# Optimization experiments

Measured on AMD Instinct MI355X. Metric: run time of the kernel, lower is better.

The kernel has to match this reference:

```python
import jax, jax.numpy as jnp
import numpy as np

N_NODES = 50000
NEG_SLOPE = 0.2
EPS = 1e-16


def _gat_layer(x, src, dst, W, a_src, a_dst, b, concat):
    """One PyG-style GATConv layer (eval mode, self-loops already in src/dst).
    x: [N, F_in], W: [F_in, H*C], a_src/a_dst: [H, C], b: [H*C] or [C].
    """
    H, C = a_src.shape
    N = x.shape[0]
    h = (x @ W).reshape(N, H, C)                      # [N, H, C]
    alpha_s = jnp.einsum('nhc,hc->nh', h, a_src)      # [N, H]
    alpha_d = jnp.einsum('nhc,hc->nh', h, a_dst)      # [N, H]
    e = alpha_s[src] + alpha_d[dst]                   # [E, H]
    e = jax.nn.leaky_relu(e, NEG_SLOPE)
    # segment softmax over edges grouped by destination node
    m = jax.ops.segment_max(e, dst, num_segments=N)   # [N, H]
    e = jnp.exp(e - m[dst])
    denom = jax.ops.segment_sum(e, dst, num_segments=N)
    alpha = e / (denom[dst] + EPS)                    # [E, H]
    msg = h[src] * alpha[:, :, None]                  # [E, H, C]
    out = jax.ops.segment_sum(msg, dst, num_segments=N)  # [N, H, C]
    if concat:
        out = out.reshape(N, H * C)
    else:
        out = out.mean(axis=1)
    return out + b


def setup_inputs() -> dict:
    key = jax.random.key(0)
    ks = jax.random.split(key, 16)
    N, E = N_NODES, 800000
    in_dim, hid, heads = 128, 64, 2
    x = jax.random.normal(ks[0], (N, in_dim), dtype=jnp.float32)
    edge_index = jax.random.randint(ks[1], (2, E), 0, N, dtype=jnp.int64)
    s = 0.1
    return {
        'x': x,
        'edge_index': edge_index,
        # layer 0: in_dim -> hid, heads
        'W0': s * jax.random.normal(ks[2], (in_dim, heads * hid), dtype=jnp.float32),
        'as0': s * jax.random.normal(ks[3], (heads, hid), dtype=jnp.float32),
        'ad0': s * jax.random.normal(ks[4], (heads, hid), dtype=jnp.float32),
        'b0': jnp.zeros((heads * hid,), dtype=jnp.float32),
        # layer 1: hid*heads -> hid, heads
        'W1': s * jax.random.normal(ks[5], (heads * hid, heads * hid), dtype=jnp.float32),
        'as1': s * jax.random.normal(ks[6], (heads, hid), dtype=jnp.float32),
        'ad1': s * jax.random.normal(ks[7], (heads, hid), dtype=jnp.float32),
        'b1': jnp.zeros((heads * hid,), dtype=jnp.float32),
        # layer 2: hid*heads -> hid, heads=1
        'W2': s * jax.random.normal(ks[8], (heads * hid, hid), dtype=jnp.float32),
        'as2': s * jax.random.normal(ks[9], (1, hid), dtype=jnp.float32),
        'ad2': s * jax.random.normal(ks[10], (1, hid), dtype=jnp.float32),
        'b2': jnp.zeros((hid,), dtype=jnp.float32),
    }


def reference(x, edge_index, W0, as0, ad0, b0, W1, as1, ad1, b1, W2, as2, ad2, b2):
    N = x.shape[0]
    # PyG GATConv default add_self_loops=True
    loop = jnp.arange(N, dtype=edge_index.dtype)
    src = jnp.concatenate([edge_index[0], loop])
    dst = jnp.concatenate([edge_index[1], loop])
    h = _gat_layer(x, src, dst, W0, as0, ad0, b0, concat=True)
    h = jax.nn.relu(h)
    h = _gat_layer(h, src, dst, W1, as1, ad1, b1, concat=True)
    h = jax.nn.relu(h)
    out = _gat_layer(h, src, dst, W2, as2, ad2, b2, concat=True)  # heads=1: concat == identity
    return out
```

## Files before the change

kernel.cpp:

```cpp
#include <hip/hip_runtime.h>
#include <hip/hip_fp16.h>

#define NEG_SLOPE 0.2f
#define EPSF 1e-16f

template<int BN, int HEADS, bool OUTH, typename XT>
__global__ __launch_bounds__(256) void gemm_fused(const XT* __restrict__ X,
                                                  const float* __restrict__ W,
                                                  const float* __restrict__ asrc,
                                                  const float* __restrict__ adst,
                                                  float* __restrict__ OutF,
                                                  __half* __restrict__ OutH,
                                                  float* __restrict__ AS,
                                                  float* __restrict__ AD, int N) {
    constexpr int BM = 64, BK = 32, K = 128;
    constexpr int TN = BN / 16;
    __shared__ float Xs[BM][BK + 4];
    __shared__ float Ws[BK][BN];
    const int tid = threadIdx.x;
    const int tx = tid & 15, ty = tid >> 4;
    const int row0 = blockIdx.x * BM;

    float acc[4][TN];
#pragma unroll
    for (int i = 0; i < 4; ++i)
#pragma unroll
        for (int j = 0; j < TN; ++j) acc[i][j] = 0.f;

    for (int kb = 0; kb < K; kb += BK) {
        __syncthreads();
        for (int idx = tid; idx < BK * (BN / 4); idx += 256) {
            int r = idx / (BN / 4), c4 = idx % (BN / 4);
            ((float4*)&Ws[r][0])[c4] = ((const float4*)&W[(size_t)(kb + r) * BN])[c4];
        }
        for (int t = tid; t < BM * (BK / 4); t += 256) {
            int r = t >> 3, c4 = t & 7;
            int gr = row0 + r;
            float f[4] = {0.f, 0.f, 0.f, 0.f};
            if (gr < N) {
                if constexpr (sizeof(XT) == 2) {
                    uint2 raw = *((const uint2*)&X[(size_t)gr * K + kb + c4 * 4]);
                    const __half2* hp = (const __half2*)&raw;
                    float2 f0 = __half22float2(hp[0]);
                    float2 f1 = __half22float2(hp[1]);
                    f[0] = f0.x; f[1] = f0.y; f[2] = f1.x; f[3] = f1.y;
                } else {
                    float4 v = *((const float4*)&X[(size_t)gr * K + kb + c4 * 4]);
                    f[0] = v.x; f[1] = v.y; f[2] = v.z; f[3] = v.w;
                }
            }
            Xs[r][c4 * 4 + 0] = f[0]; Xs[r][c4 * 4 + 1] = f[1];
            Xs[r][c4 * 4 + 2] = f[2]; Xs[r][c4 * 4 + 3] = f[3];
        }
        __syncthreads();
#pragma unroll
        for (int k = 0; k < BK; ++k) {
            float xr[4];
#pragma unroll
            for (int i = 0; i < 4; ++i) xr[i] = Xs[ty * 4 + i][k];
            float wv[TN];
#pragma unroll
            for (int j4 = 0; j4 < TN / 4; ++j4) {
                float4 w4 = ((float4*)&Ws[k][0])[tx * (TN / 4) + j4];
                wv[j4 * 4 + 0] = w4.x; wv[j4 * 4 + 1] = w4.y;
                wv[j4 * 4 + 2] = w4.z; wv[j4 * 4 + 3] = w4.w;
            }
#pragma unroll
            for (int i = 0; i < 4; ++i)
#pragma unroll
                for (int j = 0; j < TN; ++j) acc[i][j] = fmaf(xr[i], wv[j], acc[i][j]);
        }
    }

    float av[TN], dv[TN];
#pragma unroll
    for (int j = 0; j < TN; ++j) { av[j] = asrc[tx * TN + j]; dv[j] = adst[tx * TN + j]; }

#pragma unroll
    for (int i = 0; i < 4; ++i) {
        int gr = row0 + ty * 4 + i;
        if (gr >= N) continue;
        if (OUTH) {
            __half2 hp[TN / 2];
#pragma unroll
            for (int j2 = 0; j2 < TN / 2; ++j2)
                hp[j2] = __floats2half2_rn(acc[i][j2 * 2], acc[i][j2 * 2 + 1]);
            if (TN == 8)
                *((uint4*)&OutH[(size_t)gr * BN + tx * TN]) = *(uint4*)hp;
            else
                *((uint2*)&OutH[(size_t)gr * BN + tx * TN]) = *(uint2*)hp;
        } else {
#pragma unroll
            for (int j4 = 0; j4 < TN / 4; ++j4) {
                float4 o4 = make_float4(acc[i][j4 * 4 + 0], acc[i][j4 * 4 + 1],
                                        acc[i][j4 * 4 + 2], acc[i][j4 * 4 + 3]);
                *((float4*)&OutF[(size_t)gr * BN + tx * TN + j4 * 4]) = o4;
            }
        }
        float ps = 0.f, pd = 0.f;
#pragma unroll
        for (int j = 0; j < TN; ++j) { ps = fmaf(acc[i][j], av[j], ps); pd = fmaf(acc[i][j], dv[j], pd); }
        if (HEADS == 2) {
            for (int o = 1; o < 8; o <<= 1) { ps += __shfl_xor(ps, o, 64); pd += __shfl_xor(pd, o, 64); }
            if ((tx & 7) == 0) { AS[gr * 2 + (tx >> 3)] = ps; AD[gr * 2 + (tx >> 3)] = pd; }
        } else {
            for (int o = 1; o < 16; o <<= 1) { ps += __shfl_xor(ps, o, 64); pd += __shfl_xor(pd, o, 64); }
            if (tx == 0) { AS[gr] = ps; AD[gr] = pd; }
        }
    }
}

__global__ void zero_kernel(int* __restrict__ p, int n4) {
    int i = blockIdx.x * blockDim.x + threadIdx.x;
    if (i < n4) ((int4*)p)[i] = make_int4(0, 0, 0, 0);
}

__global__ void hist_kernel(const int* __restrict__ ei, int E_raw, int N,
                            int* __restrict__ cnt) {
    const int E = E_raw + N;
    for (int e = blockIdx.x * blockDim.x + threadIdx.x; e < E; e += gridDim.x * blockDim.x) {
        int d = (e < E_raw) ? ei[E_raw + e] : e - E_raw;
        atomicAdd(&cnt[d], 1);
    }
}

__global__ __launch_bounds__(256) void scan_block(const int* __restrict__ cnt,
                                                  int* __restrict__ offs,
                                                  int* __restrict__ bsum, int N) {
    __shared__ int wsum[4];
    const int i = blockIdx.x * 256 + threadIdx.x;
    const int lane = threadIdx.x & 63, w = threadIdx.x >> 6;
    int v = (i < N) ? cnt[i] : 0;
    int incl = v;
    for (int o = 1; o < 64; o <<= 1) {
        int t = __shfl_up(incl, o, 64);
        if (lane >= o) incl += t;
    }
    if (lane == 63) wsum[w] = incl;
    __syncthreads();
    int prefix = 0;
    for (int k = 0; k < w; ++k) prefix += wsum[k];
    if (i < N) offs[i] = prefix + incl - v;
    if (threadIdx.x == 255) bsum[blockIdx.x] = prefix + incl;
}

__global__ __launch_bounds__(256) void scan_bsum(int* __restrict__ bsum, int nb) {
    __shared__ int wsum[4];
    const int lane = threadIdx.x & 63, w = threadIdx.x >> 6;
    int v = (threadIdx.x < nb) ? bsum[threadIdx.x] : 0;
    int incl = v;
    for (int o = 1; o < 64; o <<= 1) {
        int t = __shfl_up(incl, o, 64);
        if (lane >= o) incl += t;
    }
    if (lane == 63) wsum[w] = incl;
    __syncthreads();
    int prefix = 0;
    for (int k = 0; k < w; ++k) prefix += wsum[k];
    if (threadIdx.x < nb) bsum[threadIdx.x] = prefix + incl - v;
}

__global__ void scan_add(int* __restrict__ offs, const int* __restrict__ bsum,
                         int N, int E) {
    const int i = blockIdx.x * 256 + threadIdx.x;
    if (i < N) offs[i] += bsum[blockIdx.x];
    if (i == 0) offs[N] = E;
}

__global__ void scatter_edges_part(const int* __restrict__ ei, int E_raw, int N,
                                   int* __restrict__ cnt,
                                   const int* __restrict__ offs,
                                   int* __restrict__ csr_src) {
    const int NPART = 8;
    const int part = blockIdx.x & (NPART - 1);
    const int gblocks = gridDim.x >> 3;
    const int grank = blockIdx.x >> 3;
    const int tid = grank * blockDim.x + threadIdx.x;
    const int nthr = gblocks * blockDim.x;
    const int E = E_raw + N;
    const int dlo = (int)(((long long)N * part) / NPART);
    const int dhi = (int)(((long long)N * (part + 1)) / NPART);
    for (int e = tid; e < E; e += nthr) {
        int d = (e < E_raw) ? ei[E_raw + e] : e - E_raw;
        if (d >= dlo && d < dhi) {
            int s = (e < E_raw) ? ei[e] : d;
            int old = atomicSub(&cnt[d], 1);
            csr_src[offs[d] + old - 1] = s;
        }
    }
}

__global__ __launch_bounds__(256) void gat_csr2(const int* __restrict__ offs,
                                                const int* __restrict__ csr_src,
                                                const float* __restrict__ AS,
                                                const float* __restrict__ AD,
                                                const __half* __restrict__ H,
                                                const float* __restrict__ bias,
                                                __half* __restrict__ Out,
                                                int N, int do_relu) {
    __shared__ int   sS[4][64];
    __shared__ float sP0[4][64];
    __shared__ float sP1[4][64];
    const int lane = threadIdx.x & 63;
    const int w = threadIdx.x >> 6;
    const int wid = (int)((blockIdx.x * blockDim.x + threadIdx.x) >> 6);
    const int nw = (int)((gridDim.x * blockDim.x) >> 6);
    const int c = lane & 15;
    const int slot = lane >> 4;
    const int myh = c >> 3;
    int* const sSw = &sS[w][0];
    const float* const myp = myh ? &sP1[w][0] : &sP0[w][0];
    const float4 bA = *(const float4*)&bias[8 * c];
    const float4 bB = *(const float4*)&bias[8 * c + 4];

    for (int n = wid; n < N; n += nw) {
        const int s0 = offs[n], s1 = offs[n + 1];
        const int deg = s1 - s0;
        const float2 adv = *(const float2*)&AD[(size_t)n * 2];
        float dn0 = 0.f, dn1 = 0.f, p0 = 0.f, p1 = 0.f;
        int sreg = 0;
        for (int i = s0 + lane; i < s1; i += 64) {
            int s = csr_src[i];
            float2 a2 = *(const float2*)&AS[(size_t)s * 2];
            float e0 = a2.x + adv.x, e1 = a2.y + adv.y;
            e0 = e0 > 0.f ? e0 : NEG_SLOPE * e0;
            e1 = e1 > 0.f ? e1 : NEG_SLOPE * e1;
            float pe0 = __expf(e0), pe1 = __expf(e1);
            dn0 += pe0; dn1 += pe1;
            if (i == s0 + lane) { sreg = s; p0 = pe0; p1 = pe1; }
        }
        for (int o = 1; o < 64; o <<= 1) {
            dn0 += __shfl_xor(dn0, o, 64);
            dn1 += __shfl_xor(dn1, o, 64);
        }
        const float myinv = 1.f / ((myh ? dn1 : dn0) + EPSF);

        float a[8];
#pragma unroll
        for (int j = 0; j < 8; ++j) a[j] = 0.f;
        if (deg <= 64) {
            sSw[lane] = sreg;
            sP0[w][lane] = p0;
            sP1[w][lane] = p1;
            const int npc = (deg + 3) >> 2;
            int t = 0;
            for (; t + 4 <= npc; t += 4) {
                int ss[4]; float pw[4]; uint4 hv[4];
#pragma unroll
                for (int k = 0; k < 4; ++k) {
                    int idx = 4 * (t + k) + slot;
                    ss[k] = sSw[idx];
                    pw[k] = myp[idx];
                }
#pragma unroll
                for (int k = 0; k < 4; ++k)
                    hv[k] = *(const uint4*)&H[(size_t)ss[k] * 128 + 8 * c];
#pragma unroll
                for (int k = 0; k < 4; ++k) {
                    const __half2* h2 = (const __half2*)&hv[k];
#pragma unroll
                    for (int j = 0; j < 4; ++j) {
                        float2 f = __half22float2(h2[j]);
                        a[2 * j]     = fmaf(f.x, pw[k], a[2 * j]);
                        a[2 * j + 1] = fmaf(f.y, pw[k], a[2 * j + 1]);
                    }
                }
            }
            for (; t < npc; ++t) {
                int idx = 4 * t + slot;
                int s = sSw[idx];
                float pw = myp[idx];
                uint4 hv = *(const uint4*)&H[(size_t)s * 128 + 8 * c];
                const __half2* h2 = (const __half2*)&hv;
#pragma unroll
                for (int j = 0; j < 4; ++j) {
                    float2 f = __half22float2(h2[j]);
                    a[2 * j]     = fmaf(f.x, pw, a[2 * j]);
                    a[2 * j + 1] = fmaf(f.y, pw, a[2 * j + 1]);
                }
            }
        } else {
            const float advh = myh ? adv.y : adv.x;
            for (int i = s0 + slot; i < s1; i += 4) {
                int s = csr_src[i];
                float e = AS[(size_t)s * 2 + myh] + advh;
                e = e > 0.f ? e : NEG_SLOPE * e;
                float pw = __expf(e);
                uint4 hv = *(const uint4*)&H[(size_t)s * 128 + 8 * c];
                const __half2* h2 = (const __half2*)&hv;
#pragma unroll
                for (int j = 0; j < 4; ++j) {
                    float2 f = __half22float2(h2[j]);
                    a[2 * j]     = fmaf(f.x, pw, a[2 * j]);
                    a[2 * j + 1] = fmaf(f.y, pw, a[2 * j + 1]);
                }
            }
        }
#pragma unroll
        for (int j = 0; j < 8; ++j) {
            a[j] += __shfl_xor(a[j], 16, 64);
            a[j] += __shfl_xor(a[j], 32, 64);
        }
        if (lane < 16) {
            float o[8];
            o[0] = a[0] * myinv + bA.x; o[1] = a[1] * myinv + bA.y;
            o[2] = a[2] * myinv + bA.z; o[3] = a[3] * myinv + bA.w;
            o[4] = a[4] * myinv + bB.x; o[5] = a[5] * myinv + bB.y;
            o[6] = a[6] * myinv + bB.z; o[7] = a[7] * myinv + bB.w;
            if (do_relu) {
#pragma unroll
                for (int j = 0; j < 8; ++j) o[j] = fmaxf(o[j], 0.f);
            }
            __half2 hp[4];
#pragma unroll
            for (int j = 0; j < 4; ++j) hp[j] = __floats2half2_rn(o[2 * j], o[2 * j + 1]);
            *(uint4*)&Out[(size_t)n * 128 + 8 * c] = *(uint4*)hp;
        }
    }
}

__global__ __launch_bounds__(256) void gat_csr1(const int* __restrict__ offs,
                                                const int* __restrict__ csr_src,
                                                const float* __restrict__ AS,
                                                const float* __restrict__ AD,
                                                const __half* __restrict__ H,
                                                const float* __restrict__ bias,
                                                float* __restrict__ Out,
                                                int N, int do_relu) {
    __shared__ int   sS[4][64];
    __shared__ float sP[4][64];
    const int lane = threadIdx.x & 63;
    const int w = threadIdx.x >> 6;
    const int wid = (int)((blockIdx.x * blockDim.x + threadIdx.x) >> 6);
    const int nw = (int)((gridDim.x * blockDim.x) >> 6);
    const int c = lane & 15;
    const int slot = lane >> 4;
    int* const sSw = &sS[w][0];
    float* const sPw = &sP[w][0];
    const float4 b4 = *(const float4*)&bias[4 * c];

    for (int n = wid; n < N; n += nw) {
        const int s0 = offs[n], s1 = offs[n + 1];
        const int deg = s1 - s0;
        const float adv0 = AD[n];
        float dn0 = 0.f, p0 = 0.f;
        int sreg = 0;
        for (int i = s0 + lane; i < s1; i += 64) {
            int s = csr_src[i];
            float e0 = AS[s] + adv0;
            e0 = e0 > 0.f ? e0 : NEG_SLOPE * e0;
            float pe0 = __expf(e0);
            dn0 += pe0;
            if (i == s0 + lane) { sreg = s; p0 = pe0; }
        }
        for (int o = 1; o < 64; o <<= 1) dn0 += __shfl_xor(dn0, o, 64);
        const float inv0 = 1.f / (dn0 + EPSF);

        float a[4];
#pragma unroll
        for (int j = 0; j < 4; ++j) a[j] = 0.f;
        if (deg <= 64) {
            sSw[lane] = sreg;
            sPw[lane] = p0;
            const int npc = (deg + 3) >> 2;
            int t = 0;
            for (; t + 4 <= npc; t += 4) {
                int ss[4]; float pw[4]; uint2 hv[4];
#pragma unroll
                for (int k = 0; k < 4; ++k) {
                    int idx = 4 * (t + k) + slot;
                    ss[k] = sSw[idx];
                    pw[k] = sPw[idx];
                }
#pragma unroll
                for (int k = 0; k < 4; ++k)
                    hv[k] = *(const uint2*)&H[(size_t)ss[k] * 64 + 4 * c];
#pragma unroll
                for (int k = 0; k < 4; ++k) {
                    const __half2* h2 = (const __half2*)&hv[k];
                    float2 f01 = __half22float2(h2[0]);
                    float2 f23 = __half22float2(h2[1]);
                    a[0] = fmaf(f01.x, pw[k], a[0]);
                    a[1] = fmaf(f01.y, pw[k], a[1]);
                    a[2] = fmaf(f23.x, pw[k], a[2]);
                    a[3] = fmaf(f23.y, pw[k], a[3]);
                }
            }
            for (; t < npc; ++t) {
                int idx = 4 * t + slot;
                int s = sSw[idx];
                float pw = sPw[idx];
                uint2 hv = *(const uint2*)&H[(size_t)s * 64 + 4 * c];
                const __half2* h2 = (const __half2*)&hv;
                float2 f01 = __half22float2(h2[0]);
                float2 f23 = __half22float2(h2[1]);
                a[0] = fmaf(f01.x, pw, a[0]);
                a[1] = fmaf(f01.y, pw, a[1]);
                a[2] = fmaf(f23.x, pw, a[2]);
                a[3] = fmaf(f23.y, pw, a[3]);
            }
        } else {
            for (int i = s0 + slot; i < s1; i += 4) {
                int s = csr_src[i];
                float e = AS[s] + adv0;
                e = e > 0.f ? e : NEG_SLOPE * e;
                float pw = __expf(e);
                uint2 hv = *(const uint2*)&H[(size_t)s * 64 + 4 * c];
                const __half2* h2 = (const __half2*)&hv;
                float2 f01 = __half22float2(h2[0]);
                float2 f23 = __half22float2(h2[1]);
                a[0] = fmaf(f01.x, pw, a[0]);
                a[1] = fmaf(f01.y, pw, a[1]);
                a[2] = fmaf(f23.x, pw, a[2]);
                a[3] = fmaf(f23.y, pw, a[3]);
            }
        }
#pragma unroll
        for (int j = 0; j < 4; ++j) {
            a[j] += __shfl_xor(a[j], 16, 64);
            a[j] += __shfl_xor(a[j], 32, 64);
        }
        if (lane < 16) {
            float4 o;
            o.x = a[0] * inv0 + b4.x;
            o.y = a[1] * inv0 + b4.y;
            o.z = a[2] * inv0 + b4.z;
            o.w = a[3] * inv0 + b4.w;
            if (do_relu) {
                o.x = fmaxf(o.x, 0.f); o.y = fmaxf(o.y, 0.f);
                o.z = fmaxf(o.z, 0.f); o.w = fmaxf(o.w, 0.f);
            }
            *(float4*)&Out[(size_t)n * 64 + 4 * c] = o;
        }
    }
}

extern "C" void kernel_launch(void* const* d_in, const int* in_sizes, int n_in,
                              void* d_out, int out_size, void* d_ws, size_t ws_size,
                              hipStream_t stream) {
    const float* x   = (const float*)d_in[0];
    const int*   ei  = (const int*)d_in[1];
    const float* W0  = (const float*)d_in[2];
    const float* as0 = (const float*)d_in[3];
    const float* ad0 = (const float*)d_in[4];
    const float* b0  = (const float*)d_in[5];
    const float* W1  = (const float*)d_in[6];
    const float* as1 = (const float*)d_in[7];
    const float* ad1 = (const float*)d_in[8];
    const float* b1  = (const float*)d_in[9];
    const float* W2  = (const float*)d_in[10];
    const float* as2 = (const float*)d_in[11];
    const float* ad2 = (const float*)d_in[12];
    const float* b2  = (const float*)d_in[13];

    const int N = in_sizes[0] / 128;
    const int E_raw = in_sizes[1] / 2;
    const int E = E_raw + N;

    char* ws = (char*)d_ws;
    size_t off = 0;
    auto alloc = [&](size_t bytes) {
        void* p = ws + off;
        off = (off + bytes + 255) & ~(size_t)255;
        return p;
    };
    __half* hh    = (__half*)alloc((size_t)N * 128 * 2);
    __half* obufh = (__half*)alloc((size_t)N * 128 * 2);
    float* asb  = (float*)alloc((size_t)N * 2 * 4);
    float* adb  = (float*)alloc((size_t)N * 2 * 4);
    int*   cnt  = (int*)alloc((size_t)(N + 4) * 4);
    int*   offs = (int*)alloc((size_t)(N + 1) * 4);
    int*   bsum = (int*)alloc(1024);
    int* csr_src = (int*)alloc((size_t)E * 4);
    (void)ws_size; (void)n_in; (void)out_size;

    const int nb = (N + 255) / 256;
    const int n4 = (N + 3) / 4;
    zero_kernel<<<(n4 + 255) / 256, 256, 0, stream>>>(cnt, n4);
    hist_kernel<<<2048, 256, 0, stream>>>(ei, E_raw, N, cnt);
    scan_block<<<nb, 256, 0, stream>>>(cnt, offs, bsum, N);
    scan_bsum<<<1, 256, 0, stream>>>(bsum, nb);
    scan_add<<<nb, 256, 0, stream>>>(offs, bsum, N, E);
    scatter_edges_part<<<2048, 256, 0, stream>>>(ei, E_raw, N, cnt, offs, csr_src);

    const int gemm_blocks = (N + 63) / 64;
    const int gat_blocks = (N * 64 + 255) / 256;

    gemm_fused<128, 2, true, float><<<gemm_blocks, 256, 0, stream>>>(x, W0, as0, ad0, nullptr, hh, asb, adb, N);
    gat_csr2<<<gat_blocks, 256, 0, stream>>>(offs, csr_src, asb, adb, hh, b0, obufh, N, 1);
    gemm_fused<128, 2, true, __half><<<gemm_blocks, 256, 0, stream>>>(obufh, W1, as1, ad1, nullptr, hh, asb, adb, N);
    gat_csr2<<<gat_blocks, 256, 0, stream>>>(offs, csr_src, asb, adb, hh, b1, obufh, N, 1);
    gemm_fused<64, 1, true, __half><<<gemm_blocks, 256, 0, stream>>>(obufh, W2, as2, ad2, nullptr, hh, asb, adb, N);
    gat_csr1<<<gat_blocks, 256, 0, stream>>>(offs, csr_src, asb, adb, hh, b2, (float*)d_out, N, 0);
}
```

Measured before the change: 277.7 us.

## Process two destination nodes per wavefront using half-wave partitioning in GAT aggregation

Splits each 64-lane wavefront into two 32-lane halves, each handling its own destination node, in both GAT aggregation kernels. The softmax pass now strides by 32 and reduces over 32 lanes, the shared-memory fast path covers degree up to 32, and each half gathers with 2 edge slots unrolled by 8. The goal is to stop wasting lanes, since average degree (about 17) leaves most of a full wavefront idle. In exchange, high-degree nodes fall to the slower path more often, and the two halves can diverge when their degrees differ.

```diff
diff --git a/kernel.cpp b/kernel.cpp
--- a/kernel.cpp
+++ b/kernel.cpp
@@ -205,21 +205,31 @@
     const int w = threadIdx.x >> 6;
     const int wid = (int)((blockIdx.x * blockDim.x + threadIdx.x) >> 6);
     const int nw = (int)((gridDim.x * blockDim.x) >> 6);
-    const int c = lane & 15;
-    const int slot = lane >> 4;
+    const int half = lane >> 5;
+    const int hl = lane & 31;
+    const int c = hl & 15;
+    const int slot = hl >> 4;
     const int myh = c >> 3;
+    const int hbase = half * 32;
     int* const sSw = &sS[w][0];
     const float* const myp = myh ? &sP1[w][0] : &sP0[w][0];
     const float4 bA = *(const float4*)&bias[8 * c];
     const float4 bB = *(const float4*)&bias[8 * c + 4];
-
-    for (int n = wid; n < N; n += nw) {
-        const int s0 = offs[n], s1 = offs[n + 1];
+    const int npairs = (N + 1) >> 1;
+
+    for (int np = wid; np < npairs; np += nw) {
+        const int n = 2 * np + half;
+        const bool active = (n < N);
+        int s0 = 0, s1 = 0;
+        float2 adv = make_float2(0.f, 0.f);
+        if (active) {
+            s0 = offs[n]; s1 = offs[n + 1];
+            adv = *(const float2*)&AD[(size_t)n * 2];
+        }
         const int deg = s1 - s0;
-        const float2 adv = *(const float2*)&AD[(size_t)n * 2];
         float dn0 = 0.f, dn1 = 0.f, p0 = 0.f, p1 = 0.f;
         int sreg = 0;
-        for (int i = s0 + lane; i < s1; i += 64) {
+        for (int i = s0 + hl; i < s1; i += 32) {
             int s = csr_src[i];
             float2 a2 = *(const float2*)&AS[(size_t)s * 2];
             float e0 = a2.x + adv.x, e1 = a2.y + adv.y;
@@ -227,9 +237,9 @@
             e1 = e1 > 0.f ? e1 : NEG_SLOPE * e1;
             float pe0 = __expf(e0), pe1 = __expf(e1);
             dn0 += pe0; dn1 += pe1;
-            if (i == s0 + lane) { sreg = s; p0 = pe0; p1 = pe1; }
-        }
-        for (int o = 1; o < 64; o <<= 1) {
+            if (i == s0 + hl) { sreg = s; p0 = pe0; p1 = pe1; }
+        }
+        for (int o = 1; o < 32; o <<= 1) {
             dn0 += __shfl_xor(dn0, o, 64);
             dn1 += __shfl_xor(dn1, o, 64);
         }
@@ -238,25 +248,25 @@
         float a[8];
 #pragma unroll
         for (int j = 0; j < 8; ++j) a[j] = 0.f;
-        if (deg <= 64) {
+        if (deg <= 32) {
             sSw[lane] = sreg;
             sP0[w][lane] = p0;
             sP1[w][lane] = p1;
-            const int npc = (deg + 3) >> 2;
+            const int npc = (deg + 1) >> 1;
             int t = 0;
-            for (; t + 4 <= npc; t += 4) {
-                int ss[4]; float pw[4]; uint4 hv[4];
-#pragma unroll
-                for (int k = 0; k < 4; ++k) {
-                    int idx = 4 * (t + k) + slot;
+            for (; t + 8 <= npc; t += 8) {
+                int ss[8]; float pw[8]; uint4 hv[8];
+#pragma unroll
+                for (int k = 0; k < 8; ++k) {
+                    int idx = hbase + 2 * (t + k) + slot;
                     ss[k] = sSw[idx];
                     pw[k] = myp[idx];
                 }
 #pragma unroll
-                for (int k = 0; k < 4; ++k)
+                for (int k = 0; k < 8; ++k)
                     hv[k] = *(const uint4*)&H[(size_t)ss[k] * 128 + 8 * c];
 #pragma unroll
-                for (int k = 0; k < 4; ++k) {
+                for (int k = 0; k < 8; ++k) {
                     const __half2* h2 = (const __half2*)&hv[k];
 #pragma unroll
                     for (int j = 0; j < 4; ++j) {
@@ -267,7 +277,7 @@
                 }
             }
             for (; t < npc; ++t) {
-                int idx = 4 * t + slot;
+                int idx = hbase + 2 * t + slot;
                 int s = sSw[idx];
                 float pw = myp[idx];
                 uint4 hv = *(const uint4*)&H[(size_t)s * 128 + 8 * c];
@@ -279,9 +289,9 @@
                     a[2 * j + 1] = fmaf(f.y, pw, a[2 * j + 1]);
                 }
             }
-        } else {
+        } else if (active) {
             const float advh = myh ? adv.y : adv.x;
-            for (int i = s0 + slot; i < s1; i += 4) {
+            for (int i = s0 + slot; i < s1; i += 2) {
                 int s = csr_src[i];
                 float e = AS[(size_t)s * 2 + myh] + advh;
                 e = e > 0.f ? e : NEG_SLOPE * e;
@@ -297,11 +307,8 @@
             }
         }
 #pragma unroll
-        for (int j = 0; j < 8; ++j) {
-            a[j] += __shfl_xor(a[j], 16, 64);
-            a[j] += __shfl_xor(a[j], 32, 64);
-        }
-        if (lane < 16) {
+        for (int j = 0; j < 8; ++j) a[j] += __shfl_xor(a[j], 16, 64);
+        if (hl < 16 && active) {
             float o[8];
             o[0] = a[0] * myinv + bA.x; o[1] = a[1] * myinv + bA.y;
             o[2] = a[2] * myinv + bA.z; o[3] = a[3] * myinv + bA.w;
@@ -333,50 +340,57 @@
     const int w = threadIdx.x >> 6;
     const int wid = (int)((blockIdx.x * blockDim.x + threadIdx.x) >> 6);
     const int nw = (int)((gridDim.x * blockDim.x) >> 6);
-    const int c = lane & 15;
-    const int slot = lane >> 4;
+    const int half = lane >> 5;
+    const int hl = lane & 31;
+    const int c = hl & 15;
+    const int slot = hl >> 4;
+    const int hbase = half * 32;
     int* const sSw = &sS[w][0];
     float* const sPw = &sP[w][0];
     const float4 b4 = *(const float4*)&bias[4 * c];
-
-    for (int n = wid; n < N; n += nw) {
-        const int s0 = offs[n], s1 = offs[n + 1];
+    const int npairs = (N + 1) >> 1;
+
+    for (int np = wid; np < npairs; np += nw) {
+        const int n = 2 * np + half;
+        const bool active = (n < N);
+        int s0 = 0, s1 = 0;
+        float adv0 = 0.f;
+        if (active) { s0 = offs[n]; s1 = offs[n + 1]; adv0 = AD[n]; }
         const int deg = s1 - s0;
-        const float adv0 = AD[n];
         float dn0 = 0.f, p0 = 0.f;
         int sreg = 0;
-        for (int i = s0 + lane; i < s1; i += 64) {
+        for (int i = s0 + hl; i < s1; i += 32) {
             int s = csr_src[i];
             float e0 = AS[s] + adv0;
             e0 = e0 > 0.f ? e0 : NEG_SLOPE * e0;
             float pe0 = __expf(e0);
             dn0 += pe0;
-            if (i == s0 + lane) { sreg = s; p0 = pe0; }
-        }
-        for (int o = 1; o < 64; o <<= 1) dn0 += __shfl_xor(dn0, o, 64);
+            if (i == s0 + hl) { sreg = s; p0 = pe0; }
+        }
+        for (int o = 1; o < 32; o <<= 1) dn0 += __shfl_xor(dn0, o, 64);
         const float inv0 = 1.f / (dn0 + EPSF);
 
         float a[4];
 #pragma unroll
         for (int j = 0; j < 4; ++j) a[j] = 0.f;
-        if (deg <= 64) {
+        if (deg <= 32) {
             sSw[lane] = sreg;
             sPw[lane] = p0;
-            const int npc = (deg + 3) >> 2;
+            const int npc = (deg + 1) >> 1;
             int t = 0;
-            for (; t + 4 <= npc; t += 4) {
-                int ss[4]; float pw[4]; uint2 hv[4];
-#pragma unroll
-                for (int k = 0; k < 4; ++k) {
-                    int idx = 4 * (t + k) + slot;
+            for (; t + 8 <= npc; t += 8) {
+                int ss[8]; float pw[8]; uint2 hv[8];
+#pragma unroll
+                for (int k = 0; k < 8; ++k) {
+                    int idx = hbase + 2 * (t + k) + slot;
                     ss[k] = sSw[idx];
                     pw[k] = sPw[idx];
                 }
 #pragma unroll
-                for (int k = 0; k < 4; ++k)
+                for (int k = 0; k < 8; ++k)
                     hv[k] = *(const uint2*)&H[(size_t)ss[k] * 64 + 4 * c];
 #pragma unroll
-                for (int k = 0; k < 4; ++k) {
+                for (int k = 0; k < 8; ++k) {
                     const __half2* h2 = (const __half2*)&hv[k];
                     float2 f01 = __half22float2(h2[0]);
                     float2 f23 = __half22float2(h2[1]);
@@ -387,7 +401,7 @@
                 }
             }
             for (; t < npc; ++t) {
-                int idx = 4 * t + slot;
+                int idx = hbase + 2 * t + slot;
                 int s = sSw[idx];
                 float pw = sPw[idx];
                 uint2 hv = *(const uint2*)&H[(size_t)s * 64 + 4 * c];
@@ -399,8 +413,8 @@
                 a[2] = fmaf(f23.x, pw, a[2]);
                 a[3] = fmaf(f23.y, pw, a[3]);
             }
-        } else {
-            for (int i = s0 + slot; i < s1; i += 4) {
+        } else if (active) {
+            for (int i = s0 + slot; i < s1; i += 2) {
                 int s = csr_src[i];
                 float e = AS[s] + adv0;
                 e = e > 0.f ? e : NEG_SLOPE * e;
@@ -416,11 +430,8 @@
             }
         }
 #pragma unroll
-        for (int j = 0; j < 4; ++j) {
-            a[j] += __shfl_xor(a[j], 16, 64);
-            a[j] += __shfl_xor(a[j], 32, 64);
-        }
-        if (lane < 16) {
+        for (int j = 0; j < 4; ++j) a[j] += __shfl_xor(a[j], 16, 64);
+        if (hl < 16 && active) {
             float4 o;
             o.x = a[0] * inv0 + b4.x;
             o.y = a[1] * inv0 + b4.y;
@@ -484,7 +495,8 @@
     scatter_edges_part<<<2048, 256, 0, stream>>>(ei, E_raw, N, cnt, offs, csr_src);
 
     const int gemm_blocks = (N + 63) / 64;
-    const int gat_blocks = (N * 64 + 255) / 256;
+    const int npairs = (N + 1) / 2;
+    const int gat_blocks = (npairs * 64 + 255) / 256;
 
     gemm_fused<128, 2, true, float><<<gemm_blocks, 256, 0, stream>>>(x, W0, as0, ad0, nullptr, hh, asb, adb, N);
     gat_csr2<<<gat_blocks, 256, 0, stream>>>(offs, csr_src, asb, adb, hh, b0, obufh, N, 1);
```

Measured after the change: 303.9 us. 1.09x slower.
